# Kernel tuning notes

Measured on AMD Instinct MI355X. Metric: run time of the kernel, lower is better.

The kernel has to match this reference:

```python
import jax, jax.numpy as jnp
import numpy as np
import math

V, E, H, L, HID, T, B = 32000, 1024, 16, 4, 4096, 1024, 4
HS = E // H  # head size = 64


def _ln(x, g, b, eps=1e-5):
    m = jnp.mean(x, axis=-1, keepdims=True)
    v = jnp.var(x, axis=-1, keepdims=True)
    return (x - m) * jax.lax.rsqrt(v + eps) * g + b


def _pos_encoding(t, e):
    pos = jnp.arange(t, dtype=jnp.float32)[:, None]
    div = jnp.exp(jnp.arange(0, e, 2, dtype=jnp.float32) * (-math.log(10000.0) / e))
    pe = jnp.zeros((t, e), dtype=jnp.float32)
    pe = pe.at[:, 0::2].set(jnp.sin(pos * div))
    pe = pe.at[:, 1::2].set(jnp.cos(pos * div))
    return pe


def setup_inputs() -> dict:
    key = jax.random.key(0)
    ks = jax.random.split(key, 16)
    std = 0.02
    inp = {
        'idx': jax.random.randint(ks[0], (B, T), 0, V),
        'targets': jax.random.randint(ks[1], (B, T), 0, V),
        'tok_emb': jax.random.normal(ks[2], (V, E), jnp.float32) * std,
        'ln1_g': jnp.ones((L, E), jnp.float32),
        'ln1_b': jnp.zeros((L, E), jnp.float32),
        'wq': jax.random.normal(ks[3], (L, H, E, HS), jnp.float32) * std,
        'wk': jax.random.normal(ks[4], (L, H, E, HS), jnp.float32) * std,
        'wv': jax.random.normal(ks[5], (L, H, E, HS), jnp.float32) * std,
        'wo': jax.random.normal(ks[6], (L, H * HS, E), jnp.float32) * std,
        'bo': jnp.zeros((L, E), jnp.float32),
        'ln2_g': jnp.ones((L, E), jnp.float32),
        'ln2_b': jnp.zeros((L, E), jnp.float32),
        'w1': jax.random.normal(ks[7], (L, E, HID), jnp.float32) * std,
        'b1': jnp.zeros((L, HID), jnp.float32),
        'w2': jax.random.normal(ks[8], (L, HID, E), jnp.float32) * std,
        'b2': jnp.zeros((L, E), jnp.float32),
        'lnf_g': jnp.ones((E,), jnp.float32),
        'lnf_b': jnp.zeros((E,), jnp.float32),
        'lm_w': jax.random.normal(ks[9], (E, V), jnp.float32) * std,
        'lm_b': jnp.zeros((V,), jnp.float32),
    }
    return inp


def _forward(idx, targets, tok_emb, ln1_g, ln1_b, wq, wk, wv, wo, bo,
             ln2_g, ln2_b, w1, b1, w2, b2, lnf_g, lnf_b, lm_w, lm_b):
    b, t = idx.shape
    x = tok_emb[idx] * math.sqrt(E)              # [B,T,E], scaled embedding
    x = x + _pos_encoding(t, E)                  # sinusoidal pos enc
    causal = jnp.tril(jnp.ones((t, t), dtype=bool))
    scale = HS ** -0.5
    for l in range(L):
        h = _ln(x, ln1_g[l], ln1_b[l])
        q = jnp.einsum('bte,hek->bhtk', h, wq[l])
        k = jnp.einsum('bte,hek->bhtk', h, wk[l])
        v = jnp.einsum('bte,hek->bhtk', h, wv[l])
        scores = jnp.einsum('bhtk,bhsk->bhts', q, k) * scale
        scores = jnp.where(causal, scores, -jnp.inf)
        w = jax.nn.softmax(scores, axis=-1)
        o = jnp.einsum('bhts,bhsk->bhtk', w, v)
        o = o.transpose(0, 2, 1, 3).reshape(b, t, H * HS)  # concat heads
        x = x + o @ wo[l] + bo[l]
        h2 = _ln(x, ln2_g[l], ln2_b[l])
        x = x + jax.nn.relu(h2 @ w1[l] + b1[l]) @ w2[l] + b2[l]
    x = _ln(x, lnf_g, lnf_b)
    logits = x @ lm_w + lm_b                     # [B,T,V]
    logp = jax.nn.log_softmax(logits, axis=-1)
    loss = -jnp.mean(jnp.take_along_axis(logp, targets[..., None], axis=-1))
    return logits, loss


def reference(idx, targets, tok_emb, ln1_g, ln1_b, wq, wk, wv, wo, bo,
              ln2_g, ln2_b, w1, b1, w2, b2, lnf_g, lnf_b, lm_w, lm_b):
    return _forward(idx, targets, tok_emb, ln1_g, ln1_b, wq, wk, wv, wo, bo,
                    ln2_g, ln2_b, w1, b1, w2, b2, lnf_g, lnf_b, lm_w, lm_b)
```

## Files before the change

kernel.cpp:

```cpp
#include <hip/hip_runtime.h>
#include <hip/hip_bf16.h>
#include <math.h>

#define BB 4
#define TT 1024
#define BT 4096
#define EE 1024
#define HH 16
#define HSZ 64
#define LL 4
#define HID 4096
#define VV 32000
#define LOG2E 1.44269504f

typedef __attribute__((ext_vector_type(8))) __bf16 bf16x8;
typedef __attribute__((ext_vector_type(4))) float f32x4;

#define MFMA16(a, b, c) __builtin_amdgcn_mfma_f32_16x16x32_bf16((a), (b), (c), 0, 0, 0)

__device__ __forceinline__ int swz32(int row, int chunk) {
    return row * 32 + ((chunk ^ ((row >> 1) & 3)) << 3);
}

__device__ __forceinline__ void gload16(const __bf16* g, __bf16* l) {
    __builtin_amdgcn_global_load_lds(
        (const __attribute__((address_space(1))) unsigned int*)g,
        (__attribute__((address_space(3))) unsigned int*)l, 16, 0, 0);
}

__global__ __launch_bounds__(256) void transpose_conv(
    const float* __restrict__ in, __bf16* __restrict__ out,
    int R, int C, long ibs, int bdiv, long os1, long os2)
{
    __shared__ __bf16 tile[64][65];
    const int t = threadIdx.x;
    const int c0 = blockIdx.x * 64, r0 = blockIdx.y * 64;
    const int batch = blockIdx.z;
    const float* ib = in + (size_t)batch * ibs;
    __bf16* ob = out + (size_t)(batch / bdiv) * os1 + (size_t)(batch % bdiv) * os2;
#pragma unroll
    for (int p = 0; p < 4; ++p) {
        const int r = (t >> 4) + p * 16;
        const int c = (t & 15) * 4;
        float4 v = *(const float4*)(ib + (size_t)(r0 + r) * C + c0 + c);
        tile[c + 0][r] = (__bf16)v.x;
        tile[c + 1][r] = (__bf16)v.y;
        tile[c + 2][r] = (__bf16)v.z;
        tile[c + 3][r] = (__bf16)v.w;
    }
    __syncthreads();
#pragma unroll
    for (int p = 0; p < 2; ++p) {
        const int g = t + p * 256;
        const int co = g >> 3, ch = g & 7;
        bf16x8 vv;
#pragma unroll
        for (int j = 0; j < 8; ++j) vv[j] = tile[co][ch * 8 + j];
        *(bf16x8*)(ob + (size_t)(c0 + co) * R + r0 + ch * 8) = vv;
    }
}

__global__ __launch_bounds__(256) void embed_kernel(
    const int* __restrict__ idx, const float* __restrict__ emb, float* __restrict__ x)
{
    const int row = blockIdx.x, tid = threadIdx.x;
    const float pos = (float)(row & (TT - 1));
    const int tok = idx[row];
    const int cb = tid * 4;
    float4 ev = *(const float4*)(emb + (size_t)tok * EE + cb);
    const float kk = -9.2103403720f / (float)EE;
    float pe[4];
#pragma unroll
    for (int j = 0; j < 4; ++j) {
        const int c = cb + j;
        const float div = expf(kk * (float)(c & ~1));
        const float ang = pos * div;
        pe[j] = (c & 1) ? cosf(ang) : sinf(ang);
    }
    float4 r;
    r.x = ev.x * 32.0f + pe[0];
    r.y = ev.y * 32.0f + pe[1];
    r.z = ev.z * 32.0f + pe[2];
    r.w = ev.w * 32.0f + pe[3];
    *(float4*)(x + (size_t)row * EE + cb) = r;
}

__global__ __launch_bounds__(256) void ln_kernel(
    const float* __restrict__ x, const float* __restrict__ g,
    const float* __restrict__ be, __bf16* __restrict__ out)
{
    __shared__ float red[2][4];
    const int row = blockIdx.x, tid = threadIdx.x;
    float4 v = *(const float4*)(x + (size_t)row * EE + tid * 4);
    float s = v.x + v.y + v.z + v.w;
    float ss = v.x * v.x + v.y * v.y + v.z * v.z + v.w * v.w;
#pragma unroll
    for (int m = 1; m < 64; m <<= 1) { s += __shfl_xor(s, m); ss += __shfl_xor(ss, m); }
    if ((tid & 63) == 0) { red[0][tid >> 6] = s; red[1][tid >> 6] = ss; }
    __syncthreads();
    s  = red[0][0] + red[0][1] + red[0][2] + red[0][3];
    ss = red[1][0] + red[1][1] + red[1][2] + red[1][3];
    const float mean = s * (1.0f / EE);
    const float var  = ss * (1.0f / EE) - mean * mean;
    const float rs   = rsqrtf(var + 1e-5f);
    float4 gv = *(const float4*)(g + tid * 4);
    float4 bv = *(const float4*)(be + tid * 4);
    __bf16* o = out + (size_t)row * EE + tid * 4;
    o[0] = (__bf16)((v.x - mean) * rs * gv.x + bv.x);
    o[1] = (__bf16)((v.y - mean) * rs * gv.y + bv.y);
    o[2] = (__bf16)((v.z - mean) * rs * gv.z + bv.z);
    o[3] = (__bf16)((v.w - mean) * rs * gv.w + bv.w);
}

template <int MODE, int BN>
__global__ __launch_bounds__(256, 2) void gemm_bt(
    const __bf16* __restrict__ A, const __bf16* __restrict__ Bt,
    const float* __restrict__ bias, float* __restrict__ C,
    __bf16* __restrict__ Cb, int M, int N, int K)
{
    constexpr int JW  = BN / 32;
    constexpr int BSW = BN / 64;
    __shared__ __bf16 As[128 * 32];
    __shared__ __bf16 Bs[BN * 32];

    const int tid = threadIdx.x;
    const int lane = tid & 63, wid = tid >> 6;
    const int wr = wid >> 1, wc = wid & 1;
    const int m0 = blockIdx.y * 128, n0 = blockIdx.x * BN;

    size_t sA[2];  int loA[2];
#pragma unroll
    for (int c = 0; c < 2; ++c) {
        const int seg = wid * 2 + c;
        const int rl = seg * 16 + (lane >> 2);
        const int cl = (lane & 3) ^ ((rl >> 1) & 3);
        loA[c] = seg * 512;
        sA[c] = (size_t)(m0 + rl) * K + cl * 8;
    }
    size_t sB[BSW]; int loB[BSW];
#pragma unroll
    for (int c = 0; c < BSW; ++c) {
        const int seg = wid * BSW + c;
        const int rl = seg * 16 + (lane >> 2);
        const int cl = (lane & 3) ^ ((rl >> 1) & 3);
        loB[c] = seg * 512;
        sB[c] = (size_t)(n0 + rl) * K + cl * 8;
    }

    const int l15 = lane & 15, kch = lane >> 4;
    const int abase = swz32(wr * 64 + l15, kch);
    const int bbase = swz32(wc * (BN / 2) + l15, kch);

    f32x4 acc[4][JW] = {};

    const int nk = K >> 5;
    for (int kt = 0; kt < nk; ++kt) {
        const size_t ko = (size_t)kt * 32;
#pragma unroll
        for (int c = 0; c < 2; ++c)   gload16(A + sA[c] + ko, As + loA[c]);
#pragma unroll
        for (int c = 0; c < BSW; ++c) gload16(Bt + sB[c] + ko, Bs + loB[c]);
        __syncthreads();
        bf16x8 af[4], bfr[JW];
#pragma unroll
        for (int i = 0; i < 4; ++i)  af[i]  = *(const bf16x8*)(As + abase + i * 512);
#pragma unroll
        for (int j = 0; j < JW; ++j) bfr[j] = *(const bf16x8*)(Bs + bbase + j * 512);
#pragma unroll
        for (int i = 0; i < 4; ++i)
#pragma unroll
            for (int j = 0; j < JW; ++j)
                acc[i][j] = MFMA16(af[i], bfr[j], acc[i][j]);
        __syncthreads();
    }

    const int crow = m0 + wr * 64 + ((lane >> 4) << 2);
    const int ccol = n0 + wc * (BN / 2) + l15;
#pragma unroll
    for (int i = 0; i < 4; ++i)
#pragma unroll
        for (int j = 0; j < JW; ++j) {
            const int cc = ccol + j * 16;
#pragma unroll
            for (int r = 0; r < 4; ++r) {
                const size_t oidx = (size_t)(crow + i * 16 + r) * N + cc;
                float v = acc[i][j][r];
                if (MODE == 0) {
                    Cb[oidx] = (__bf16)v;
                } else if (MODE == 1) {
                    v += bias[cc];
                    Cb[oidx] = (__bf16)(v > 0.0f ? v : 0.0f);
                } else if (MODE == 2) {
                    C[oidx] += v + bias[cc];
                } else {
                    C[oidx] = v + bias[cc];
                }
            }
        }
}

template <int MODE, int GSWZ>
__global__ __launch_bounds__(512, 2) void gemm_bt2(
    const __bf16* __restrict__ A, const __bf16* __restrict__ Bt,
    const float* __restrict__ bias, float* __restrict__ C,
    __bf16* __restrict__ Cb, float2* __restrict__ part,
    int M, int N, int K)
{
    __shared__ __bf16 As[256 * 32];
    __shared__ __bf16 Bs[128 * 32];
    __shared__ float2 red[(MODE == 4) ? 256 : 1][2];

    const int tid = threadIdx.x;
    const int lane = tid & 63, wid = tid >> 6;
    const int wm = wid >> 1, wn = wid & 1;
    int bm, bn;
    if (GSWZ) {
        const int b = blockIdx.x;
        const int j = b >> 3;
        bm = (b & 7) * 2 + (j & 1);
        bn = j >> 1;
    } else {
        bm = blockIdx.y; bn = blockIdx.x;
    }
    const int m0 = bm * 256, n0 = bn * 128;
    const int l15 = lane & 15, lg = lane >> 4;

    size_t sA[2];  int loA[2];
#pragma unroll
    for (int c = 0; c < 2; ++c) {
        const int seg = wid * 2 + c;
        const int rl = seg * 16 + (lane >> 2);
        const int cl = (lane & 3) ^ ((rl >> 1) & 3);
        loA[c] = seg * 512;
        sA[c] = (size_t)(m0 + rl) * K + cl * 8;
    }
    size_t sB;  int loB;
    {
        const int rl = wid * 16 + (lane >> 2);
        const int cl = (lane & 3) ^ ((rl >> 1) & 3);
        loB = wid * 512;
        sB = (size_t)(n0 + rl) * K + cl * 8;
    }

    const int abase = swz32(wm * 64 + l15, lg);
    const int bbase = swz32(wn * 64 + l15, lg);

    f32x4 acc[4][4] = {};

    const int nk = K >> 5;
    for (int kt = 0; kt < nk; ++kt) {
        const size_t ko = (size_t)kt * 32;
        gload16(A + sA[0] + ko, As + loA[0]);
        gload16(A + sA[1] + ko, As + loA[1]);
        gload16(Bt + sB + ko, Bs + loB);
        __syncthreads();
        bf16x8 af[4], bfr[4];
#pragma unroll
        for (int i = 0; i < 4; ++i) af[i]  = *(const bf16x8*)(As + abase + i * 512);
#pragma unroll
        for (int j = 0; j < 4; ++j) bfr[j] = *(const bf16x8*)(Bs + bbase + j * 512);
#pragma unroll
        for (int i = 0; i < 4; ++i)
#pragma unroll
            for (int j = 0; j < 4; ++j)
                acc[i][j] = MFMA16(af[i], bfr[j], acc[i][j]);
        __syncthreads();
    }

    const int crow = m0 + wm * 64 + lg * 4;
    const int ccol = n0 + wn * 64 + l15;
#pragma unroll
    for (int i = 0; i < 4; ++i)
#pragma unroll
        for (int j = 0; j < 4; ++j) {
            const int cc = ccol + j * 16;
#pragma unroll
            for (int r = 0; r < 4; ++r) {
                const size_t oidx = (size_t)(crow + i * 16 + r) * N + cc;
                float v = acc[i][j][r];
                if (MODE == 0) {
                    Cb[oidx] = (__bf16)v;
                } else if (MODE == 1) {
                    v += bias[cc];
                    Cb[oidx] = (__bf16)(v > 0.0f ? v : 0.0f);
                } else {
                    C[oidx] = v + bias[cc];
                }
            }
        }

    if constexpr (MODE == 4) {
#pragma unroll
        for (int i = 0; i < 4; ++i)
#pragma unroll
            for (int r = 0; r < 4; ++r) {
                float tv[4];
                float mx = -1e30f;
#pragma unroll
                for (int j = 0; j < 4; ++j) {
                    tv[j] = acc[i][j][r] + bias[ccol + j * 16];
                    mx = fmaxf(mx, tv[j]);
                }
                mx = fmaxf(mx, __shfl_xor(mx, 1));
                mx = fmaxf(mx, __shfl_xor(mx, 2));
                mx = fmaxf(mx, __shfl_xor(mx, 4));
                mx = fmaxf(mx, __shfl_xor(mx, 8));
                float sm = 0.0f;
#pragma unroll
                for (int j = 0; j < 4; ++j) sm += exp2f((tv[j] - mx) * LOG2E);
                sm += __shfl_xor(sm, 1);
                sm += __shfl_xor(sm, 2);
                sm += __shfl_xor(sm, 4);
                sm += __shfl_xor(sm, 8);
                if (l15 == 0)
                    red[wm * 64 + i * 16 + lg * 4 + r][wn] = make_float2(mx, sm);
            }
        __syncthreads();
        if (tid < 256) {
            const float2 a = red[tid][0], b2 = red[tid][1];
            const float M2 = fmaxf(a.x, b2.x);
            const float S = a.y * exp2f((a.x - M2) * LOG2E)
                          + b2.y * exp2f((b2.x - M2) * LOG2E);
            part[(size_t)(m0 + tid) * (N >> 7) + bn] = make_float2(M2, S);
        }
    }
}

__global__ __launch_bounds__(64) void attn_kernel(
    const __bf16* __restrict__ qkv, __bf16* __restrict__ out)
{
    __shared__ __bf16 Pl[16 * 32];
    __shared__ __bf16 Vt[64 * 32];
    const int lane = threadIdx.x;
    const int bh = blockIdx.x, b = bh >> 4, hh = bh & 15;
    const int qbase = blockIdx.y * 16;
    const int RS = 3 * EE;
    const __bf16* qp = qkv + (size_t)(b * TT) * RS + hh * HSZ;
    const __bf16* kp = qp + EE;
    const __bf16* vp = qp + 2 * EE;
    const int l15 = lane & 15, lg = lane >> 4;

    bf16x8 aq[2];
#pragma unroll
    for (int e = 0; e < 2; ++e)
        aq[e] = *(const bf16x8*)(qp + (size_t)(qbase + l15) * RS + e * 32 + lg * 8);

    f32x4 ao[4] = {};
    float mrun[4], lrun[4];
#pragma unroll
    for (int r = 0; r < 4; ++r) { mrun[r] = -1e30f; lrun[r] = 0.0f; }

    const int ntile = qbase / 32 + 1;
    for (int st = 0; st < ntile; ++st) {
        const int sbase = st * 32;
        f32x4 as[2] = {};
        __builtin_amdgcn_s_setprio(1);
#pragma unroll
        for (int n = 0; n < 2; ++n)
#pragma unroll
            for (int e = 0; e < 2; ++e) {
                bf16x8 bk = *(const bf16x8*)(kp + (size_t)(sbase + n * 16 + l15) * RS + e * 32 + lg * 8);
                as[n] = MFMA16(aq[e], bk, as[n]);
            }
        __builtin_amdgcn_s_setprio(0);
        {
            const int sl = lane >> 1;
            const int e0 = (lane & 1) * 32;
            const __bf16* vr = vp + (size_t)(sbase + sl) * RS + e0;
#pragma unroll
            for (int c = 0; c < 4; ++c) {
                bf16x8 vvv = *(const bf16x8*)(vr + c * 8);
#pragma unroll
                for (int j = 0; j < 8; ++j)
                    Vt[swz32(e0 + c * 8 + j, sl >> 3) + (sl & 7)] = vvv[j];
            }
        }
#pragma unroll
        for (int r = 0; r < 4; ++r) {
            const int qi = qbase + lg * 4 + r;
            float sc0 = as[0][r] * 0.125f;
            float sc1 = as[1][r] * 0.125f;
            if (sbase + l15 > qi)      sc0 = -1e30f;
            if (sbase + 16 + l15 > qi) sc1 = -1e30f;
            float rm = fmaxf(sc0, sc1);
            rm = fmaxf(rm, __shfl_xor(rm, 1));
            rm = fmaxf(rm, __shfl_xor(rm, 2));
            rm = fmaxf(rm, __shfl_xor(rm, 4));
            rm = fmaxf(rm, __shfl_xor(rm, 8));
            const float mnew = fmaxf(mrun[r], rm);
            const float alpha = exp2f((mrun[r] - mnew) * LOG2E);
            const float p0 = exp2f((sc0 - mnew) * LOG2E);
            const float p1 = exp2f((sc1 - mnew) * LOG2E);
            float rs = p0 + p1;
            rs += __shfl_xor(rs, 1);
            rs += __shfl_xor(rs, 2);
            rs += __shfl_xor(rs, 4);
            rs += __shfl_xor(rs, 8);
            lrun[r] = lrun[r] * alpha + rs;
            mrun[r] = mnew;
#pragma unroll
            for (int n = 0; n < 4; ++n) ao[n][r] *= alpha;
            const int prow = lg * 4 + r;
            Pl[swz32(prow, l15 >> 3) + (l15 & 7)] = (__bf16)p0;
            Pl[swz32(prow, (16 + l15) >> 3) + (l15 & 7)] = (__bf16)p1;
        }
        asm volatile("s_waitcnt lgkmcnt(0)" ::: "memory");
        bf16x8 pa = *(const bf16x8*)(&Pl[swz32(l15, lg)]);
        __builtin_amdgcn_s_setprio(1);
#pragma unroll
        for (int n = 0; n < 4; ++n) {
            bf16x8 bv = *(const bf16x8*)(&Vt[swz32(n * 16 + l15, lg)]);
            ao[n] = MFMA16(pa, bv, ao[n]);
        }
        __builtin_amdgcn_s_setprio(0);
        asm volatile("s_waitcnt lgkmcnt(0)" ::: "memory");
    }
#pragma unroll
    for (int r = 0; r < 4; ++r) {
        const float inv = 1.0f / lrun[r];
        const int row = qbase + lg * 4 + r;
#pragma unroll
        for (int n = 0; n < 4; ++n)
            out[(size_t)(b * TT + row) * EE + hh * HSZ + n * 16 + l15] =
                (__bf16)(ao[n][r] * inv);
    }
}

__global__ __launch_bounds__(256) void loss_reduce(
    const float2* __restrict__ part, const float* __restrict__ logits,
    const int* __restrict__ tgt, float* __restrict__ lossv, int NP)
{
    __shared__ float rm[4], rs2[4];
    const int row = blockIdx.x, tid = threadIdx.x;
    float m = -1e30f, s = 0.0f;
    if (tid < NP) {
        const float2 p = part[(size_t)row * NP + tid];
        m = p.x; s = p.y;
    }
#pragma unroll
    for (int k = 1; k < 64; k <<= 1) {
        const float mo = __shfl_xor(m, k), so = __shfl_xor(s, k);
        const float mn = fmaxf(m, mo);
        s = s * exp2f((m - mn) * LOG2E) + so * exp2f((mo - mn) * LOG2E);
        m = mn;
    }
    if ((tid & 63) == 0) { rm[tid >> 6] = m; rs2[tid >> 6] = s; }
    __syncthreads();
    if (tid == 0) {
        float M = rm[0];
#pragma unroll
        for (int w = 1; w < 4; ++w) M = fmaxf(M, rm[w]);
        float S = 0.0f;
#pragma unroll
        for (int w = 0; w < 4; ++w) S += rs2[w] * exp2f((rm[w] - M) * LOG2E);
        lossv[row] = M + logf(S) - logits[(size_t)row * VV + tgt[row]];
    }
}

__global__ __launch_bounds__(256) void loss_final(const float* __restrict__ lossv, float* __restrict__ out)
{
    __shared__ float red[4];
    const int tid = threadIdx.x;
    float s = 0.0f;
    for (int i = tid; i < BT; i += 256) s += lossv[i];
#pragma unroll
    for (int k = 1; k < 64; k <<= 1) s += __shfl_xor(s, k);
    if ((tid & 63) == 0) red[tid >> 6] = s;
    __syncthreads();
    if (tid == 0) out[0] = (red[0] + red[1] + red[2] + red[3]) * (1.0f / BT);
}

extern "C" void kernel_launch(void* const* d_in, const int* in_sizes, int n_in,
                              void* d_out, int out_size, void* d_ws, size_t ws_size,
                              hipStream_t stream)
{
    const int*   idx   = (const int*)d_in[0];
    const int*   tgt   = (const int*)d_in[1];
    const float* temb  = (const float*)d_in[2];
    const float* ln1g  = (const float*)d_in[3];
    const float* ln1b  = (const float*)d_in[4];
    const float* wq    = (const float*)d_in[5];
    const float* wk    = (const float*)d_in[6];
    const float* wv    = (const float*)d_in[7];
    const float* wo    = (const float*)d_in[8];
    const float* bo    = (const float*)d_in[9];
    const float* ln2g  = (const float*)d_in[10];
    const float* ln2b  = (const float*)d_in[11];
    const float* w1    = (const float*)d_in[12];
    const float* b1    = (const float*)d_in[13];
    const float* w2    = (const float*)d_in[14];
    const float* b2    = (const float*)d_in[15];
    const float* lnfg  = (const float*)d_in[16];
    const float* lnfb  = (const float*)d_in[17];
    const float* lm_w  = (const float*)d_in[18];
    const float* lm_b  = (const float*)d_in[19];

    float* logits  = (float*)d_out;
    float* lossout = logits + (size_t)BT * VV;

    char* ws = (char*)d_ws;
    size_t off = 0;
    auto carve = [&](size_t bytes) {
        void* p = ws + off;
        off += (bytes + 255) & ~(size_t)255;
        return p;
    };
    __bf16* WQKVT = (__bf16*)carve((size_t)LL * 3072 * 1024 * 2);
    __bf16* WOT   = (__bf16*)carve((size_t)LL * 1024 * 1024 * 2);
    __bf16* W1T   = (__bf16*)carve((size_t)LL * 4096 * 1024 * 2);
    __bf16* W2T   = (__bf16*)carve((size_t)LL * 1024 * 4096 * 2);
    __bf16* LMT   = (__bf16*)carve((size_t)VV * 1024 * 2);
    float*  x     = (float*)carve((size_t)BT * EE * 4);
    __bf16* h     = (__bf16*)carve((size_t)BT * EE * 2);
    __bf16* qkv   = (__bf16*)carve((size_t)BT * 3072 * 2);
    __bf16* mid   = (__bf16*)carve((size_t)BT * HID * 2);
    float*  lossv = (float*)carve((size_t)BT * 4);
    float2* part  = (float2*)mid;

    const dim3 blk(256);

    transpose_conv<<<dim3(1, 16, 64), blk, 0, stream>>>(wq, WQKVT,           1024, 64,   65536, 16, 3145728, 65536);
    transpose_conv<<<dim3(1, 16, 64), blk, 0, stream>>>(wk, WQKVT + 1048576, 1024, 64,   65536, 16, 3145728, 65536);
    transpose_conv<<<dim3(1, 16, 64), blk, 0, stream>>>(wv, WQKVT + 2097152, 1024, 64,   65536, 16, 3145728, 65536);
    transpose_conv<<<dim3(16, 16, 4), blk, 0, stream>>>(wo, WOT,   1024, 1024, 1048576, 4, 0, 1048576);
    transpose_conv<<<dim3(64, 16, 4), blk, 0, stream>>>(w1, W1T,   1024, 4096, 4194304, 4, 0, 4194304);
    transpose_conv<<<dim3(16, 64, 4), blk, 0, stream>>>(w2, W2T,   4096, 1024, 4194304, 4, 0, 4194304);
    transpose_conv<<<dim3(500, 16, 1), blk, 0, stream>>>(lm_w, LMT, 1024, 32000, 0, 1, 0, 0);

    embed_kernel<<<BT, blk, 0, stream>>>(idx, temb, x);

    for (int l = 0; l < LL; ++l) {
        ln_kernel<<<BT, blk, 0, stream>>>(x, ln1g + l * EE, ln1b + l * EE, h);
        gemm_bt2<0, 0><<<dim3(24, 16), dim3(512), 0, stream>>>(h, WQKVT + (size_t)l * 3145728,
                                                               nullptr, nullptr, qkv, nullptr, BT, 3072, 1024);
        attn_kernel<<<dim3(64, 64), dim3(64), 0, stream>>>(qkv, h);
        gemm_bt<2, 64><<<dim3(16, 32), blk, 0, stream>>>(h, WOT + (size_t)l * 1048576,
                                                         bo + l * EE, x, nullptr, BT, 1024, 1024);
        ln_kernel<<<BT, blk, 0, stream>>>(x, ln2g + l * EE, ln2b + l * EE, h);
        gemm_bt2<1, 0><<<dim3(32, 16), dim3(512), 0, stream>>>(h, W1T + (size_t)l * 4194304,
                                                               b1 + l * HID, nullptr, mid, nullptr, BT, 4096, 1024);
        gemm_bt<2, 64><<<dim3(16, 32), blk, 0, stream>>>(mid, W2T + (size_t)l * 4194304,
                                                         b2 + l * EE, x, nullptr, BT, 1024, 4096);
    }
    ln_kernel<<<BT, blk, 0, stream>>>(x, lnfg, lnfb, h);
    gemm_bt2<4, 1><<<dim3(4000), dim3(512), 0, stream>>>(h, LMT, lm_b, logits, nullptr, part, BT, VV, 1024);
    loss_reduce<<<BT, blk, 0, stream>>>(part, logits, tgt, lossv, VV >> 7);
    loss_final<<<1, blk, 0, stream>>>(lossv, lossout);
}
```

Measured before the change: 1.674 ms.

## Split attention key tiles across two waves and revert QKV/FFN1 GEMMs to gemm_bt

```diff
diff --git a/kernel.cpp b/kernel.cpp
--- a/kernel.cpp
+++ b/kernel.cpp
@@ -216,9 +216,9 @@
     int bm, bn;
     if (GSWZ) {
         const int b = blockIdx.x;
-        const int j = b >> 3;
-        bm = (b & 7) * 2 + (j & 1);
-        bn = j >> 1;
+        const int gl = (b & 7) * (gridDim.x >> 3) + (b >> 3);
+        bn = gl >> 4;
+        bm = gl & 15;
     } else {
         bm = blockIdx.y; bn = blockIdx.x;
     }
@@ -326,12 +326,13 @@
     }
 }
 
-__global__ __launch_bounds__(64) void attn_kernel(
+__global__ __launch_bounds__(128) void attn_kernel(
     const __bf16* __restrict__ qkv, __bf16* __restrict__ out)
 {
-    __shared__ __bf16 Pl[16 * 32];
-    __shared__ __bf16 Vt[64 * 32];
-    const int lane = threadIdx.x;
+    __shared__ __align__(16) char smem[2 * (16 * 32 + 64 * 32) * 2];
+    const int tid = threadIdx.x, lane = tid & 63, w = tid >> 6;
+    __bf16* Pl = (__bf16*)smem + w * (16 * 32 + 64 * 32);
+    __bf16* Vt = Pl + 16 * 32;
     const int bh = blockIdx.x, b = bh >> 4, hh = bh & 15;
     const int qbase = blockIdx.y * 16;
     const int RS = 3 * EE;
@@ -351,7 +352,7 @@
     for (int r = 0; r < 4; ++r) { mrun[r] = -1e30f; lrun[r] = 0.0f; }
 
     const int ntile = qbase / 32 + 1;
-    for (int st = 0; st < ntile; ++st) {
+    for (int st = w; st < ntile; st += 2) {
         const int sbase = st * 32;
         f32x4 as[2] = {};
         __builtin_amdgcn_s_setprio(1);
@@ -415,14 +416,39 @@
         __builtin_amdgcn_s_setprio(0);
         asm volatile("s_waitcnt lgkmcnt(0)" ::: "memory");
     }
-#pragma unroll
-    for (int r = 0; r < 4; ++r) {
-        const float inv = 1.0f / lrun[r];
-        const int row = qbase + lg * 4 + r;
-#pragma unroll
-        for (int n = 0; n < 4; ++n)
-            out[(size_t)(b * TT + row) * EE + hh * HSZ + n * 16 + l15] =
-                (__bf16)(ao[n][r] * inv);
+
+    __syncthreads();
+    float* Mb = (float*)smem;
+    float* Lb = Mb + 4 * 64;
+    f32x4* Ob = (f32x4*)(Lb + 4 * 64);
+    if (w == 1) {
+#pragma unroll
+        for (int r = 0; r < 4; ++r) { Mb[r * 64 + lane] = mrun[r]; Lb[r * 64 + lane] = lrun[r]; }
+#pragma unroll
+        for (int n = 0; n < 4; ++n) Ob[n * 64 + lane] = ao[n];
+    }
+    __syncthreads();
+    if (w == 0) {
+        float a0[4], a1[4], inv[4];
+#pragma unroll
+        for (int r = 0; r < 4; ++r) {
+            const float m1 = Mb[r * 64 + lane];
+            const float l1 = Lb[r * 64 + lane];
+            const float mm = fmaxf(mrun[r], m1);
+            a0[r] = exp2f((mrun[r] - mm) * LOG2E);
+            a1[r] = exp2f((m1 - mm) * LOG2E);
+            inv[r] = 1.0f / (lrun[r] * a0[r] + l1 * a1[r]);
+        }
+#pragma unroll
+        for (int n = 0; n < 4; ++n) {
+            const f32x4 o1 = Ob[n * 64 + lane];
+#pragma unroll
+            for (int r = 0; r < 4; ++r) {
+                const int row = qbase + lg * 4 + r;
+                out[(size_t)(b * TT + row) * EE + hh * HSZ + n * 16 + l15] =
+                    (__bf16)((ao[n][r] * a0[r] + o1[r] * a1[r]) * inv[r]);
+            }
+        }
     }
 }
 
@@ -531,14 +557,14 @@
 
     for (int l = 0; l < LL; ++l) {
         ln_kernel<<<BT, blk, 0, stream>>>(x, ln1g + l * EE, ln1b + l * EE, h);
-        gemm_bt2<0, 0><<<dim3(24, 16), dim3(512), 0, stream>>>(h, WQKVT + (size_t)l * 3145728,
-                                                               nullptr, nullptr, qkv, nullptr, BT, 3072, 1024);
-        attn_kernel<<<dim3(64, 64), dim3(64), 0, stream>>>(qkv, h);
+        gemm_bt<0, 128><<<dim3(24, 32), blk, 0, stream>>>(h, WQKVT + (size_t)l * 3145728,
+                                                          nullptr, nullptr, qkv, BT, 3072, 1024);
+        attn_kernel<<<dim3(64, 64), dim3(128), 0, stream>>>(qkv, h);
         gemm_bt<2, 64><<<dim3(16, 32), blk, 0, stream>>>(h, WOT + (size_t)l * 1048576,
                                                          bo + l * EE, x, nullptr, BT, 1024, 1024);
         ln_kernel<<<BT, blk, 0, stream>>>(x, ln2g + l * EE, ln2b + l * EE, h);
-        gemm_bt2<1, 0><<<dim3(32, 16), dim3(512), 0, stream>>>(h, W1T + (size_t)l * 4194304,
-                                                               b1 + l * HID, nullptr, mid, nullptr, BT, 4096, 1024);
+        gemm_bt<1, 128><<<dim3(32, 32), blk, 0, stream>>>(h, W1T + (size_t)l * 4194304,
+                                                          b1 + l * HID, nullptr, mid, BT, 4096, 1024);
         gemm_bt<2, 64><<<dim3(16, 32), blk, 0, stream>>>(mid, W2T + (size_t)l * 4194304,
                                                          b2 + l * EE, x, nullptr, BT, 1024, 4096);
     }
```

Measured after the change: 1.721 ms. 1.03x slower.
